# Kernel tuning notes

Hardware: AMD Instinct MI355X
Metric: run time of the kernel (lower is better)

Reference implementation:

```python
import jax, jax.numpy as jnp
import numpy as np

B, S, H = 1, 2048, 4096
NQ, NKV, D = 32, 8, 128
N_REP = NQ // NKV
SCALE = 1.0 / np.sqrt(D)
SOFTCAP = 30.0
EPS = 1e-5


def _rotate_half(x):
    x1, x2 = jnp.split(x, 2, axis=-1)
    return jnp.concatenate([-x2, x1], axis=-1)


def _rms_norm(x, w, eps=EPS):
    xf = x.astype(jnp.float32)
    norm = xf * jax.lax.rsqrt(jnp.mean(xf * xf, axis=-1, keepdims=True) + eps)
    return (w * norm).astype(x.dtype)


def setup_inputs() -> dict:
    key = jax.random.key(0)
    ks = jax.random.split(key, 8)
    hidden_states = jax.random.normal(ks[0], (B, S, H), dtype=jnp.float32)
    # causal additive mask
    causal = jnp.tril(jnp.ones((S, S), dtype=bool))
    attention_mask = jnp.where(causal, 0.0, -1e9)[None, None].astype(jnp.float32)
    # RoPE cache
    inv_freq = 1.0 / (10000.0 ** (np.arange(0, D, 2, dtype=np.float32) / D))
    t = np.arange(S, dtype=np.float32)
    freqs = np.outer(t, inv_freq)                      # (S, D/2)
    emb = np.concatenate([freqs, freqs], axis=-1)      # (S, D)
    cos = jnp.asarray(np.cos(emb))[None, None]         # (1,1,S,D)
    sin = jnp.asarray(np.sin(emb))[None, None]
    # params
    std = 0.02
    wq = jax.random.normal(ks[1], (NQ * D, H), dtype=jnp.float32) * std
    wk = jax.random.normal(ks[2], (NKV * D, H), dtype=jnp.float32) * std
    wv = jax.random.normal(ks[3], (NKV * D, H), dtype=jnp.float32) * std
    wo = jax.random.normal(ks[4], (H, NQ * D), dtype=jnp.float32) * std
    pre_norm_w = jnp.ones((H,), dtype=jnp.float32)
    q_norm_w = jnp.ones((D,), dtype=jnp.float32)
    k_norm_w = jnp.ones((D,), dtype=jnp.float32)
    return {
        "hidden_states": hidden_states, "attention_mask": attention_mask,
        "cos": cos, "sin": sin, "pre_norm_w": pre_norm_w,
        "wq": wq, "wk": wk, "wv": wv, "wo": wo,
        "q_norm_w": q_norm_w, "k_norm_w": k_norm_w,
    }


def reference(hidden_states, attention_mask, cos, sin, pre_norm_w,
              wq, wk, wv, wo, q_norm_w, k_norm_w):
    residual = hidden_states
    h = _rms_norm(hidden_states, pre_norm_w)
    bsz, seq_len, _ = h.shape
    # projections -> (b, heads, s, d)
    q = jnp.einsum('bsh,eh->bse', h, wq).reshape(bsz, seq_len, NQ, D).transpose(0, 2, 1, 3)
    k = jnp.einsum('bsh,eh->bse', h, wk).reshape(bsz, seq_len, NKV, D).transpose(0, 2, 1, 3)
    v = jnp.einsum('bsh,eh->bse', h, wv).reshape(bsz, seq_len, NKV, D).transpose(0, 2, 1, 3)
    # QK RMSNorm over head_dim
    q = _rms_norm(q, q_norm_w)
    k = _rms_norm(k, k_norm_w)
    # RoPE (full head_dim)
    q = q * cos + _rotate_half(q) * sin
    k = k * cos + _rotate_half(k) * sin
    # GQA: repeat kv heads
    k_exp = jnp.repeat(k, N_REP, axis=1)  # (b, NQ, s, d)
    v_exp = jnp.repeat(v, N_REP, axis=1)
    scores = jnp.einsum('bhqd,bhkd->bhqk', q, k_exp) * SCALE
    scores = SOFTCAP * jnp.tanh(scores / SOFTCAP)
    scores = scores + attention_mask
    probs = jax.nn.softmax(scores.astype(jnp.float32), axis=-1).astype(q.dtype)
    attn = jnp.einsum('bhqk,bhkd->bhqd', probs, v_exp)
    attn = attn.transpose(0, 2, 1, 3).reshape(bsz, seq_len, NQ * D)
    out = jnp.einsum('bse,he->bsh', attn, wo)
    return residual + out
```

## Files before the change

### kernel.cpp

```cpp
#include <hip/hip_runtime.h>
#include <cstdint>

typedef __bf16 bf16;
typedef __bf16 bf16x8 __attribute__((ext_vector_type(8)));
typedef __bf16 bf16x4 __attribute__((ext_vector_type(4)));
typedef float  f32x4  __attribute__((ext_vector_type(4)));

#define SEQ  2048
#define HID  4096
#define DH   128
#define NQH  32
#define NKVH 8
#define NTOT 6144
#define RSCALE 0.08838834764831845f
#define SOFTCAP 30.0f
#define L2E 1.4426950408889634f

__device__ __forceinline__ void gl2lds16(const void* g, void* l) {
  __builtin_amdgcn_global_load_lds(
      (const __attribute__((address_space(1))) unsigned int*)g,
      (__attribute__((address_space(3))) unsigned int*)l, 16, 0, 0);
}

__global__ void cvt_kernel(const float* __restrict__ in, bf16* __restrict__ out, int n4) {
  const int stride = gridDim.x * blockDim.x;
  for (int i = blockIdx.x * blockDim.x + threadIdx.x; i < n4; i += stride) {
    const float4 v = ((const float4*)in)[i];
    bf16x4 o = { (bf16)v.x, (bf16)v.y, (bf16)v.z, (bf16)v.w };
    *(bf16x4*)(out + (size_t)i * 4) = o;
  }
}

__global__ void rmsnorm_kernel(const float* __restrict__ x, const float* __restrict__ w,
                               bf16* __restrict__ out) {
  const int s = blockIdx.x;
  const float* xr = x + (size_t)s * HID;
  float4 v[4];
  float ss = 0.f;
#pragma unroll
  for (int j = 0; j < 4; ++j) {
    v[j] = ((const float4*)xr)[threadIdx.x + j * 256];
    ss += v[j].x * v[j].x + v[j].y * v[j].y + v[j].z * v[j].z + v[j].w * v[j].w;
  }
#pragma unroll
  for (int m = 1; m < 64; m <<= 1) ss += __shfl_xor(ss, m);
  __shared__ float red[4];
  if ((threadIdx.x & 63) == 0) red[threadIdx.x >> 6] = ss;
  __syncthreads();
  const float rn = rsqrtf((red[0] + red[1] + red[2] + red[3]) * (1.f / HID) + 1e-5f);
  bf16* orow = out + (size_t)s * HID;
#pragma unroll
  for (int j = 0; j < 4; ++j) {
    const int idx = (threadIdx.x + j * 256) * 4;
    const float4 wv = ((const float4*)w)[threadIdx.x + j * 256];
    bf16x4 o = { (bf16)(v[j].x * rn * wv.x), (bf16)(v[j].y * rn * wv.y),
                 (bf16)(v[j].z * rn * wv.z), (bf16)(v[j].w * rn * wv.w) };
    *(bf16x4*)(orow + idx) = o;
  }
}

template<bool FINAL>
__global__ __launch_bounds__(512, 1)
void gemm8(const bf16* __restrict__ A, const bf16* __restrict__ B,
           bf16* __restrict__ Cb, float* __restrict__ Cf,
           const float* __restrict__ resid, int M, int N, int K)
{
  extern __shared__ char smem[];
  const int tid  = threadIdx.x;
  const int lane = tid & 63;
  const int wave = tid >> 6;
  const int wm = wave >> 2, wn = wave & 3;

  const int gx = gridDim.x;
  const int nwg = gx * gridDim.y;
  int lin = blockIdx.x + gx * blockIdx.y;
  lin = (lin & 7) * (nwg >> 3) + (lin >> 3);
  const int m0 = (lin / gx) * 128;
  const int n0 = (lin % gx) * 256;

  auto Abuf = [&](int b) -> bf16* { return (bf16*)(smem + b * 49152); };
  auto Bbuf = [&](int b) -> bf16* { return (bf16*)(smem + b * 49152 + 16384); };

  auto stage_half = [&](int kt, int b, int h) {
    if (h == 0) {
#pragma unroll
      for (int i = 0; i < 2; ++i) {
        const int c = wave * 2 + i;
        const int row = c * 8 + (lane >> 3);
        const int col8 = (lane & 7) ^ (row & 7);
        gl2lds16(A + (size_t)(m0 + row) * K + kt + col8 * 8, Abuf(b) + c * 512);
      }
      {
        const int c = wave * 4;
        const int row = c * 8 + (lane >> 3);
        const int col8 = (lane & 7) ^ (row & 7);
        gl2lds16(B + (size_t)(n0 + row) * K + kt + col8 * 8, Bbuf(b) + c * 512);
      }
    } else {
#pragma unroll
      for (int i = 1; i < 4; ++i) {
        const int c = wave * 4 + i;
        const int row = c * 8 + (lane >> 3);
        const int col8 = (lane & 7) ^ (row & 7);
        gl2lds16(B + (size_t)(n0 + row) * K + kt + col8 * 8, Bbuf(b) + c * 512);
      }
    }
  };

  f32x4 acc[4][4] = {};
  const int nt = K / 64;

  stage_half(0, 0, 0);  stage_half(0, 0, 1);
  stage_half(64, 1, 0); stage_half(64, 1, 1);
  asm volatile("s_waitcnt vmcnt(6)" ::: "memory");
  __builtin_amdgcn_s_barrier();

  for (int t = 0; t < nt; ++t) {
    const int cur = t % 3;
    const bf16* Ab = Abuf(cur);
    const bf16* Bb = Bbuf(cur);
    const int nxt = (t + 2) % 3;
    const bool pf = (t + 2) < nt;

#pragma unroll
    for (int ks = 0; ks < 2; ++ks) {
      bf16x8 af[4], bfv[4];
#pragma unroll
      for (int mi = 0; mi < 4; ++mi) {
        const int row = wm * 64 + mi * 16 + (lane & 15);
        const int slot = (ks * 4 + (lane >> 4)) ^ (row & 7);
        af[mi] = *(const bf16x8*)(Ab + row * 64 + slot * 8);
      }
#pragma unroll
      for (int ni = 0; ni < 4; ++ni) {
        const int row = wn * 64 + ni * 16 + (lane & 15);
        const int slot = (ks * 4 + (lane >> 4)) ^ (row & 7);
        bfv[ni] = *(const bf16x8*)(Bb + row * 64 + slot * 8);
      }
      if (pf) stage_half((t + 2) * 64, nxt, ks);

      __builtin_amdgcn_s_barrier();
      asm volatile("s_waitcnt lgkmcnt(0)" ::: "memory");
      __builtin_amdgcn_sched_barrier(0);
      __builtin_amdgcn_s_setprio(1);
#pragma unroll
      for (int mi = 0; mi < 4; ++mi)
#pragma unroll
        for (int ni = 0; ni < 4; ++ni)
          acc[mi][ni] = __builtin_amdgcn_mfma_f32_16x16x32_bf16(af[mi], bfv[ni], acc[mi][ni], 0, 0, 0);
      __builtin_amdgcn_s_setprio(0);

      if (ks == 1) {
        if (pf)                asm volatile("s_waitcnt vmcnt(6)" ::: "memory");
        else if (t + 1 < nt)   asm volatile("s_waitcnt vmcnt(0)" ::: "memory");
      }
      __builtin_amdgcn_s_barrier();
    }
  }

#pragma unroll
  for (int mi = 0; mi < 4; ++mi) {
#pragma unroll
    for (int i = 0; i < 4; ++i) {
      const int m = m0 + wm * 64 + mi * 16 + (lane >> 4) * 4 + i;
#pragma unroll
      for (int ni = 0; ni < 4; ++ni) {
        const int n = n0 + wn * 64 + ni * 16 + (lane & 15);
        const float v = acc[mi][ni][i];
        if constexpr (FINAL) {
          Cf[(size_t)m * N + n] = v + resid[(size_t)m * N + n];
        } else {
          Cb[(size_t)m * N + n] = (bf16)v;
        }
      }
    }
  }
}

__global__ void qkrope_kernel(const bf16* __restrict__ qkv,
                              const float* __restrict__ qw, const float* __restrict__ kw,
                              const float* __restrict__ cs, const float* __restrict__ sn,
                              bf16* __restrict__ qr, bf16* __restrict__ kr)
{
  const int w = blockIdx.x * 4 + (threadIdx.x >> 6);
  const int lane = threadIdx.x & 63;
  const int s = w / (NQH + NKVH);
  const int hh = w % (NQH + NKVH);
  const bf16* src; bf16* dst; const float* nw;
  if (hh < NQH) {
    src = qkv + (size_t)s * NTOT + hh * DH;
    dst = qr + ((size_t)hh * SEQ + s) * DH;
    nw = qw;
  } else {
    const int h2 = hh - NQH;
    src = qkv + (size_t)s * NTOT + 4096 + h2 * DH;
    dst = kr + ((size_t)h2 * SEQ + s) * DH;
    nw = kw;
  }
  const float x0 = (float)src[lane], x1 = (float)src[lane + 64];
  float ss = x0 * x0 + x1 * x1;
#pragma unroll
  for (int m = 1; m < 64; m <<= 1) ss += __shfl_xor(ss, m);
  const float rn = rsqrtf(ss * (1.f / DH) + 1e-5f);
  const float n0 = x0 * rn * nw[lane], n1 = x1 * rn * nw[lane + 64];
  const float c0 = cs[s * DH + lane],      s0 = sn[s * DH + lane];
  const float c1 = cs[s * DH + lane + 64], s1 = sn[s * DH + lane + 64];
  dst[lane]      = (bf16)(n0 * c0 - n1 * s0);
  dst[lane + 64] = (bf16)(n1 * c1 + n0 * s1);
}

__global__ void vtrans_kernel(const bf16* __restrict__ qkv, bf16* __restrict__ vt)
{
  __shared__ bf16 tbuf[64][33];
  const int s0 = blockIdx.x * 64;
  const int d0 = blockIdx.y * 32;
  const int h  = blockIdx.z;
  const int tid = threadIdx.x;
  {
    const int col = tid & 31, r0 = tid >> 5;
    for (int r = r0; r < 64; r += 8)
      tbuf[r][col] = qkv[(size_t)(s0 + r) * NTOT + 5120 + h * DH + d0 + col];
  }
  __syncthreads();
  {
    const int sc = tid & 63, dr0 = tid >> 6;
    for (int d = dr0; d < 32; d += 4)
      vt[((size_t)h * DH + d0 + d) * SEQ + s0 + sc] = tbuf[sc][d];
  }
}

__global__ __launch_bounds__(256, 2)
void attn_kernel(const bf16* __restrict__ Q, const bf16* __restrict__ Kr,
                 const bf16* __restrict__ Vt, bf16* __restrict__ Oa)
{
  __shared__ bf16 Ks[2][64 * 128];
  __shared__ bf16 Vs[2][128 * 64];
  __shared__ bf16 Ps[4][32 * 64];

  const int tid = threadIdx.x, lane = tid & 63, wave = tid >> 6;

  const int lin  = blockIdx.x + 16 * blockIdx.y;
  const int slot = lin >> 8, idx = lin & 255;
  const int bx   = slot ? (15 - (idx & 15)) : (idx & 15);
  const int head = (slot << 4) | (idx >> 4);
  const int kvh  = head >> 2;
  const int q0   = bx * 128;
  const int wq0  = q0 + wave * 32;

  const bf16* Qh = Q  + (size_t)head * SEQ * DH;
  const bf16* Kh = Kr + (size_t)kvh * SEQ * DH;
  const bf16* Vh = Vt + (size_t)kvh * DH * SEQ;

  bf16x8 qf[2][4];
#pragma unroll
  for (int mt = 0; mt < 2; ++mt)
#pragma unroll
    for (int kc = 0; kc < 4; ++kc) {
      const int r = wq0 + mt * 16 + (lane & 15);
      qf[mt][kc] = *(const bf16x8*)(Qh + (size_t)r * DH + kc * 32 + (lane >> 4) * 8);
    }

  float lsum[2][4] = {};
  f32x4 o_acc[2][8] = {};

  const int ntiles = q0 / 64 + 2;

  auto stage = [&](int t, int b) {
    const int kv0 = t * 64;
    bf16* Kd = &Ks[b][0];
    bf16* Vd = &Vs[b][0];
#pragma unroll
    for (int i2 = 0; i2 < 4; ++i2) {
      const int c = wave * 4 + i2;
      {
        const int row = c * 4 + (lane >> 4);
        const int col8 = (lane & 15) ^ (row & 15);
        gl2lds16(Kh + (size_t)(kv0 + row) * DH + col8 * 8, Kd + c * 512);
      }
      {
        const int row = c * 8 + (lane >> 3);
        const int col8 = (lane & 7) ^ (row & 7);
        gl2lds16(Vh + (size_t)row * SEQ + kv0 + col8 * 8, Vd + c * 512);
      }
    }
  };

  stage(0, 0);
  __syncthreads();

  const float ZS = RSCALE / SOFTCAP;
  const float A1 = RSCALE * L2E;
  const float B3 = -(ZS * ZS) * (1.f / 3.f);
  const float B5 = (2.f / 15.f) * (ZS * ZS) * (ZS * ZS);
  const float C  = SOFTCAP * L2E;

  for (int t = 0; t < ntiles; ++t) {
    const int cur = t & 1;
    if (t + 1 < ntiles) stage(t + 1, cur ^ 1);
    const int kv0 = t * 64;
    const bf16* Kb = &Ks[cur][0];
    const bf16* Vb = &Vs[cur][0];

    if (kv0 <= wq0 + 31) {
      f32x4 sc[2][4] = {};
      __builtin_amdgcn_s_setprio(1);
#pragma unroll
      for (int ks = 0; ks < 4; ++ks) {
        bf16x8 kf[4];
#pragma unroll
        for (int nt = 0; nt < 4; ++nt) {
          const int row = nt * 16 + (lane & 15);
          const int sl = (ks * 4 + (lane >> 4)) ^ (row & 15);
          kf[nt] = *(const bf16x8*)(Kb + row * 128 + sl * 8);
        }
#pragma unroll
        for (int mt = 0; mt < 2; ++mt)
#pragma unroll
          for (int nt = 0; nt < 4; ++nt)
            sc[mt][nt] = __builtin_amdgcn_mfma_f32_16x16x32_bf16(qf[mt][ks], kf[nt], sc[mt][nt], 0, 0, 0);
      }
      __builtin_amdgcn_s_setprio(0);

      if (kv0 + 63 <= wq0) {
#pragma unroll
        for (int mt = 0; mt < 2; ++mt)
#pragma unroll
          for (int i = 0; i < 4; ++i)
#pragma unroll
            for (int nt = 0; nt < 4; ++nt) {
              const float s = sc[mt][nt][i];
              const float w = s * s;
              const float poly = fmaf(fmaf(B5, w, B3), w, 1.f);
              const float p = __builtin_amdgcn_exp2f(fmaf(s * poly, A1, -C));
              sc[mt][nt][i] = p;
              lsum[mt][i] += p;
            }
      } else {
#pragma unroll
        for (int mt = 0; mt < 2; ++mt)
#pragma unroll
          for (int i = 0; i < 4; ++i) {
            const int qrow = wq0 + mt * 16 + (lane >> 4) * 4 + i;
#pragma unroll
            for (int nt = 0; nt < 4; ++nt) {
              const int col = kv0 + nt * 16 + (lane & 15);
              const float s = sc[mt][nt][i];
              const float w = s * s;
              const float poly = fmaf(fmaf(B5, w, B3), w, 1.f);
              float p = __builtin_amdgcn_exp2f(fmaf(s * poly, A1, -C));
              if (col > qrow) p = 0.f;
              sc[mt][nt][i] = p;
              lsum[mt][i] += p;
            }
          }
      }

#pragma unroll
      for (int mt = 0; mt < 2; ++mt)
#pragma unroll
        for (int nt = 0; nt < 4; ++nt)
#pragma unroll
          for (int i = 0; i < 4; ++i) {
            const int r = mt * 16 + (lane >> 4) * 4 + i;
            const int colb = nt * 16 + (lane & 15);
            const int sl = (colb >> 3) ^ (r & 7);
            Ps[wave][r * 64 + sl * 8 + (colb & 7)] = (bf16)sc[mt][nt][i];
          }
      asm volatile("s_waitcnt lgkmcnt(0)" ::: "memory");
      __builtin_amdgcn_sched_barrier(0);

      __builtin_amdgcn_s_setprio(1);
#pragma unroll
      for (int ks2 = 0; ks2 < 2; ++ks2) {
        bf16x8 pf[2];
#pragma unroll
        for (int mt = 0; mt < 2; ++mt) {
          const int r = mt * 16 + (lane & 15);
          const int sl = (ks2 * 4 + (lane >> 4)) ^ (r & 7);
          pf[mt] = *(const bf16x8*)(&Ps[wave][r * 64 + sl * 8]);
        }
#pragma unroll
        for (int nt = 0; nt < 8; ++nt) {
          const int row = nt * 16 + (lane & 15);
          const int sl = (ks2 * 4 + (lane >> 4)) ^ (row & 7);
          const bf16x8 vf = *(const bf16x8*)(Vb + row * 64 + sl * 8);
          o_acc[0][nt] = __builtin_amdgcn_mfma_f32_16x16x32_bf16(pf[0], vf, o_acc[0][nt], 0, 0, 0);
          o_acc[1][nt] = __builtin_amdgcn_mfma_f32_16x16x32_bf16(pf[1], vf, o_acc[1][nt], 0, 0, 0);
        }
      }
      __builtin_amdgcn_s_setprio(0);
    }
    __syncthreads();
  }

#pragma unroll
  for (int mt = 0; mt < 2; ++mt)
#pragma unroll
    for (int i = 0; i < 4; ++i) {
      float l = lsum[mt][i];
#pragma unroll
      for (int m = 1; m < 16; m <<= 1) l += __shfl_xor(l, m);
      const int qrow = wq0 + mt * 16 + (lane >> 4) * 4 + i;
      const float inv_l = 1.f / l;
#pragma unroll
      for (int nt = 0; nt < 8; ++nt) {
        const int d = nt * 16 + (lane & 15);
        Oa[(size_t)qrow * HID + head * DH + d] = (bf16)(o_acc[mt][nt][i] * inv_l);
      }
    }
}

extern "C" void kernel_launch(void* const* d_in, const int* in_sizes, int n_in,
                              void* d_out, int out_size, void* d_ws, size_t ws_size,
                              hipStream_t stream)
{
  const float* hidden = (const float*)d_in[0];
  const float* cosb   = (const float*)d_in[2];
  const float* sinb   = (const float*)d_in[3];
  const float* prew   = (const float*)d_in[4];
  const float* wq     = (const float*)d_in[5];
  const float* wk     = (const float*)d_in[6];
  const float* wv     = (const float*)d_in[7];
  const float* wo     = (const float*)d_in[8];
  const float* qnw    = (const float*)d_in[9];
  const float* knw    = (const float*)d_in[10];
  float* outp = (float*)d_out;
  char* ws = (char*)d_ws;

  bf16* wqkv = (bf16*)(ws + 0);
  bf16* hb   = (bf16*)(ws + 50331648);
  bf16* qkvp = (bf16*)(ws + 67108864);
  bf16* kr   = (bf16*)(ws + 92274688);
  bf16* vt   = (bf16*)(ws + 96468992);
  bf16* wob  = wqkv;

  cvt_kernel<<<2048, 256, 0, stream>>>(wq, wqkv, 4096 * HID / 4);
  cvt_kernel<<<1024, 256, 0, stream>>>(wk, wqkv + (size_t)4096 * HID, 1024 * HID / 4);
  cvt_kernel<<<1024, 256, 0, stream>>>(wv, wqkv + (size_t)5120 * HID, 1024 * HID / 4);
  rmsnorm_kernel<<<SEQ, 256, 0, stream>>>(hidden, prew, hb);

  gemm8<false><<<dim3(NTOT / 256, SEQ / 128), 512, 147456, stream>>>(
      hb, wqkv, qkvp, nullptr, nullptr, SEQ, NTOT, HID);

  cvt_kernel<<<2048, 256, 0, stream>>>(wo, wob, HID * HID / 4);

  qkrope_kernel<<<SEQ * (NQH + NKVH) / 4, 256, 0, stream>>>(qkvp, qnw, knw, cosb, sinb, hb, kr);
  vtrans_kernel<<<dim3(32, 4, 8), 256, 0, stream>>>(qkvp, vt);

  attn_kernel<<<dim3(16, 32), 256, 0, stream>>>(hb, kr, vt, qkvp);

  gemm8<true><<<dim3(HID / 256, SEQ / 128), 512, 147456, stream>>>(
      qkvp, wob, nullptr, outp, hidden, SEQ, HID, HID);
}
```

Baseline: 373.6 us.

## Enlarge GEMM tile to 256x256 with double-buffered LDS staging

Both projection GEMMs move from a 128x256 tile with a three-stage LDS pipeline to a 256x256 tile with two LDS buffers. Each wave now keeps 8x4 accumulator fragments and walks the A tile in four sub-steps, while the next K tile is staged. The intent is to raise data reuse per LDS load and halve global traffic for B. In exchange it launches half as many workgroups (192 and 128, fewer than the CU count), loses a prefetch stage, and the 512x2 launch bound tightens registers and may cause spills.

Result: slower. 396.9 us (+6.2%).

```diff
diff --git a/kernel.cpp b/kernel.cpp
--- a/kernel.cpp
+++ b/kernel.cpp
@@ -60,10 +60,10 @@
 }
 
 template<bool FINAL>
-__global__ __launch_bounds__(512, 1)
-void gemm8(const bf16* __restrict__ A, const bf16* __restrict__ B,
-           bf16* __restrict__ Cb, float* __restrict__ Cf,
-           const float* __restrict__ resid, int M, int N, int K)
+__global__ __launch_bounds__(512, 2)
+void gemm256(const bf16* __restrict__ A, const bf16* __restrict__ B,
+             bf16* __restrict__ Cb, float* __restrict__ Cf,
+             const float* __restrict__ resid, int M, int N, int K)
 {
   extern __shared__ char smem[];
   const int tid  = threadIdx.x;
@@ -75,98 +75,96 @@
   const int nwg = gx * gridDim.y;
   int lin = blockIdx.x + gx * blockIdx.y;
   lin = (lin & 7) * (nwg >> 3) + (lin >> 3);
-  const int m0 = (lin / gx) * 128;
+  const int m0 = (lin / gx) * 256;
   const int n0 = (lin % gx) * 256;
 
-  auto Abuf = [&](int b) -> bf16* { return (bf16*)(smem + b * 49152); };
-  auto Bbuf = [&](int b) -> bf16* { return (bf16*)(smem + b * 49152 + 16384); };
-
-  auto stage_half = [&](int kt, int b, int h) {
-    if (h == 0) {
-#pragma unroll
-      for (int i = 0; i < 2; ++i) {
-        const int c = wave * 2 + i;
-        const int row = c * 8 + (lane >> 3);
-        const int col8 = (lane & 7) ^ (row & 7);
-        gl2lds16(A + (size_t)(m0 + row) * K + kt + col8 * 8, Abuf(b) + c * 512);
-      }
-      {
-        const int c = wave * 4;
-        const int row = c * 8 + (lane >> 3);
-        const int col8 = (lane & 7) ^ (row & 7);
-        gl2lds16(B + (size_t)(n0 + row) * K + kt + col8 * 8, Bbuf(b) + c * 512);
-      }
-    } else {
-#pragma unroll
-      for (int i = 1; i < 4; ++i) {
-        const int c = wave * 4 + i;
-        const int row = c * 8 + (lane >> 3);
-        const int col8 = (lane & 7) ^ (row & 7);
-        gl2lds16(B + (size_t)(n0 + row) * K + kt + col8 * 8, Bbuf(b) + c * 512);
-      }
+  auto Abuf = [&](int b) -> bf16* { return (bf16*)(smem + b * 65536); };
+  auto Bbuf = [&](int b) -> bf16* { return (bf16*)(smem + b * 65536 + 32768); };
+
+  auto stage = [&](int kt, int b) {
+    bf16* Ad = Abuf(b);
+    bf16* Bd = Bbuf(b);
+#pragma unroll
+    for (int i = 0; i < 4; ++i) {
+      const int c = i * 8 + wave;
+      const int row = c * 8 + (lane >> 3);
+      const int col8 = (lane & 7) ^ (row & 7);
+      gl2lds16(A + (size_t)(m0 + row) * K + kt + col8 * 8, Ad + c * 512);
+    }
+#pragma unroll
+    for (int i = 0; i < 4; ++i) {
+      const int c = i * 8 + wave;
+      const int row = c * 8 + (lane >> 3);
+      const int col8 = (lane & 7) ^ (row & 7);
+      gl2lds16(B + (size_t)(n0 + row) * K + kt + col8 * 8, Bd + c * 512);
     }
   };
 
-  f32x4 acc[4][4] = {};
+  f32x4 acc[8][4] = {};
   const int nt = K / 64;
 
-  stage_half(0, 0, 0);  stage_half(0, 0, 1);
-  stage_half(64, 1, 0); stage_half(64, 1, 1);
-  asm volatile("s_waitcnt vmcnt(6)" ::: "memory");
+  stage(0, 0);
+  asm volatile("s_waitcnt vmcnt(0)" ::: "memory");
   __builtin_amdgcn_s_barrier();
 
   for (int t = 0; t < nt; ++t) {
-    const int cur = t % 3;
-    const bf16* Ab = Abuf(cur);
-    const bf16* Bb = Bbuf(cur);
-    const int nxt = (t + 2) % 3;
-    const bool pf = (t + 2) < nt;
-
-#pragma unroll
-    for (int ks = 0; ks < 2; ++ks) {
-      bf16x8 af[4], bfv[4];
-#pragma unroll
-      for (int mi = 0; mi < 4; ++mi) {
-        const int row = wm * 64 + mi * 16 + (lane & 15);
-        const int slot = (ks * 4 + (lane >> 4)) ^ (row & 7);
-        af[mi] = *(const bf16x8*)(Ab + row * 64 + slot * 8);
-      }
-#pragma unroll
-      for (int ni = 0; ni < 4; ++ni) {
-        const int row = wn * 64 + ni * 16 + (lane & 15);
-        const int slot = (ks * 4 + (lane >> 4)) ^ (row & 7);
-        bfv[ni] = *(const bf16x8*)(Bb + row * 64 + slot * 8);
-      }
-      if (pf) stage_half((t + 2) * 64, nxt, ks);
+    const int p = t & 1;
+    const bf16* Ab = Abuf(p);
+    const bf16* Bb = Bbuf(p);
+    bf16x8 bfr[4][2];
+
+#pragma unroll
+    for (int q = 0; q < 4; ++q) {
+      bf16x8 afr[2][2];
+#pragma unroll
+      for (int mi = 0; mi < 2; ++mi)
+#pragma unroll
+        for (int ks = 0; ks < 2; ++ks) {
+          const int row = wm * 128 + q * 32 + mi * 16 + (lane & 15);
+          const int slot = (ks * 4 + (lane >> 4)) ^ (row & 7);
+          afr[mi][ks] = *(const bf16x8*)(Ab + row * 64 + slot * 8);
+        }
+      if (q == 0) {
+#pragma unroll
+        for (int ni = 0; ni < 4; ++ni)
+#pragma unroll
+          for (int ks = 0; ks < 2; ++ks) {
+            const int row = wn * 64 + ni * 16 + (lane & 15);
+            const int slot = (ks * 4 + (lane >> 4)) ^ (row & 7);
+            bfr[ni][ks] = *(const bf16x8*)(Bb + row * 64 + slot * 8);
+          }
+        if (t + 1 < nt) stage((t + 1) * 64, p ^ 1);
+      }
 
       __builtin_amdgcn_s_barrier();
       asm volatile("s_waitcnt lgkmcnt(0)" ::: "memory");
       __builtin_amdgcn_sched_barrier(0);
       __builtin_amdgcn_s_setprio(1);
 #pragma unroll
-      for (int mi = 0; mi < 4; ++mi)
-#pragma unroll
-        for (int ni = 0; ni < 4; ++ni)
-          acc[mi][ni] = __builtin_amdgcn_mfma_f32_16x16x32_bf16(af[mi], bfv[ni], acc[mi][ni], 0, 0, 0);
+      for (int ks = 0; ks < 2; ++ks)
+#pragma unroll
+        for (int mi = 0; mi < 2; ++mi)
+#pragma unroll
+          for (int ni = 0; ni < 4; ++ni)
+            acc[q * 2 + mi][ni] = __builtin_amdgcn_mfma_f32_16x16x32_bf16(
+                afr[mi][ks], bfr[ni][ks], acc[q * 2 + mi][ni], 0, 0, 0);
       __builtin_amdgcn_s_setprio(0);
 
-      if (ks == 1) {
-        if (pf)                asm volatile("s_waitcnt vmcnt(6)" ::: "memory");
-        else if (t + 1 < nt)   asm volatile("s_waitcnt vmcnt(0)" ::: "memory");
-      }
+      if (q == 3 && t + 1 < nt)
+        asm volatile("s_waitcnt vmcnt(0)" ::: "memory");
       __builtin_amdgcn_s_barrier();
     }
   }
 
 #pragma unroll
-  for (int mi = 0; mi < 4; ++mi) {
+  for (int a = 0; a < 8; ++a) {
 #pragma unroll
     for (int i = 0; i < 4; ++i) {
-      const int m = m0 + wm * 64 + mi * 16 + (lane >> 4) * 4 + i;
+      const int m = m0 + wm * 128 + (a >> 1) * 32 + (a & 1) * 16 + (lane >> 4) * 4 + i;
 #pragma unroll
       for (int ni = 0; ni < 4; ++ni) {
         const int n = n0 + wn * 64 + ni * 16 + (lane & 15);
-        const float v = acc[mi][ni][i];
+        const float v = acc[a][ni][i];
         if constexpr (FINAL) {
           Cf[(size_t)m * N + n] = v + resid[(size_t)m * N + n];
         } else {
@@ -439,7 +437,7 @@
   cvt_kernel<<<1024, 256, 0, stream>>>(wv, wqkv + (size_t)5120 * HID, 1024 * HID / 4);
   rmsnorm_kernel<<<SEQ, 256, 0, stream>>>(hidden, prew, hb);
 
-  gemm8<false><<<dim3(NTOT / 256, SEQ / 128), 512, 147456, stream>>>(
+  gemm256<false><<<dim3(NTOT / 256, SEQ / 256), 512, 131072, stream>>>(
       hb, wqkv, qkvp, nullptr, nullptr, SEQ, NTOT, HID);
 
   cvt_kernel<<<2048, 256, 0, stream>>>(wo, wob, HID * HID / 4);
@@ -449,6 +447,6 @@
 
   attn_kernel<<<dim3(16, 32), 256, 0, stream>>>(hb, kr, vt, qkvp);
 
-  gemm8<true><<<dim3(HID / 256, SEQ / 128), 512, 147456, stream>>>(
+  gemm256<true><<<dim3(HID / 256, SEQ / 256), 512, 131072, stream>>>(
       qkvp, wob, nullptr, outp, hidden, SEQ, HID, HID);
 }
```
